# Kernel optimization log

Hardware: AMD Instinct MI355X
Metric: run time of the kernel (lower is better)

## Reference

```python
import jax, jax.numpy as jnp
import numpy as np

B, CIN, COUT, K = 8, 64, 64, 3
H, W = 256, 256
PAD = 1


def setup_inputs() -> dict:
    key = jax.random.key(0)
    k1, k2, k3, k4 = jax.random.split(key, 4)
    x = jax.random.normal(k1, (B, CIN, H, W), dtype=jnp.float32)
    alpha = jax.random.uniform(k2, (B, CIN, 1, 1), dtype=jnp.float32)
    # learned params per init_kwargs (groups=1 -> cin_per_group = CIN)
    weight = jax.random.normal(k3, (1, COUT, CIN, K, K), dtype=jnp.float32) * 0.05
    bias = jax.random.normal(k4, (1, COUT), dtype=jnp.float32) * 0.05
    return {"x": x, "alpha": alpha, "weight": weight, "bias": bias}


def reference(x, alpha, weight, bias):
    # cal_dim='cin': per-sample modulated weights
    # alpha: (B, CIN, 1, 1) -> (B, 1, CIN, 1, 1); weight: (1, COUT, CIN, K, K)
    w = alpha[:, None] * weight  # (B, COUT, CIN, K, K)

    def conv_one(xi, wi):
        # xi: (CIN, H, W), wi: (COUT, CIN, K, K)
        out = jax.lax.conv_general_dilated(
            xi[None], wi,
            window_strides=(1, 1),
            padding=[(PAD, PAD), (PAD, PAD)],
            dimension_numbers=("NCHW", "OIHW", "NCHW"),
        )
        return out[0]  # (COUT, H, W)

    out = jax.vmap(conv_one)(x, w)  # (B, COUT, H, W)
    # bias is repeated per-sample in the torch code -> same bias every sample
    return out + bias[0][None, :, None, None]
```

## Files before the change

### kernel.cpp

```cpp
#include <hip/hip_runtime.h>


typedef __attribute__((ext_vector_type(8))) short short8;
typedef __attribute__((ext_vector_type(4))) float float4v;

#define BB 8
#define CI_N 64
#define CO_N 64
#define HH 256
#define WW 256
#define HW (HH * WW)
#define TW 32
#define TH 8
#define HALO_W 34
#define HALO_H 10
#define HALO_PX (HALO_W * HALO_H)
#define RS 72
#define HI_OFF 32

#define NFRAG (2 * 9 * 2 * 4 * 64 * 8)

__device__ __forceinline__ unsigned f2bf(float v) {
    unsigned u = __float_as_uint(v);
    return (u + 0x7FFFu + ((u >> 16) & 1u)) >> 16;
}

__global__ void prepack_w(const float* __restrict__ w, ushort* __restrict__ wp) {
    int idx = blockIdx.x * 256 + threadIdx.x;
    if (idx >= NFRAG) return;
    int j     = idx & 7;
    int lane  = (idx >> 3) & 63;
    int mt    = (idx >> 9) & 3;
    int plane = (idx >> 11) & 1;
    int rest  = idx >> 12;
    int k     = rest % 9;
    int chunk = rest / 9;
    int co = mt * 16 + (lane & 15);
    int ci = chunk * 32 + (lane >> 4) * 8 + j;
    float v = w[(co * CI_N + ci) * 9 + k];
    unsigned hi = f2bf(v);
    float fhi = __uint_as_float(hi << 16);
    unsigned lo = f2bf(v - fhi);
    wp[idx] = (ushort)(plane ? lo : hi);
}

__global__ __launch_bounds__(512, 4) void conv_mfma(
    const float* __restrict__ x,
    const float* __restrict__ alpha,
    const ushort* __restrict__ wp,
    const float* __restrict__ bias,
    float* __restrict__ out)
{
    __shared__ __align__(16) ushort sx[HALO_PX * RS];

    const int tid    = threadIdx.x;
    const int lane   = tid & 63;
    const int w_id   = tid >> 6;
    const int n_lane = lane & 15;
    const int q      = lane >> 4;

    const int id  = blockIdx.x;
    const int b   = id & 7;
    const int t   = id >> 3;
    const int tx  = t & 7;
    const int ty  = t >> 3;
    const int gx0 = tx * TW;
    const int gy0 = ty * TH;

    const int m_half = w_id >> 2;
    const int n_q    = w_id & 3;

    float4v acc[2][4];
#pragma unroll
    for (int mt = 0; mt < 2; ++mt) {
        float4v bi;
#pragma unroll
        for (int r = 0; r < 4; ++r)
            bi[r] = bias[(m_half * 2 + mt) * 16 + q * 4 + r];
#pragma unroll
        for (int nt = 0; nt < 4; ++nt) acc[mt][nt] = bi;
    }

    const float* xb = x + (size_t)b * CI_N * HW;
    const int vbase = (n_q * 2 * HALO_W + n_lane) * RS + q * 8;

    int gofs[6];
    unsigned okm = 0;
#pragma unroll
    for (int it = 0; it < 6; ++it) {
        int hp = it * 64 + lane;
        int hy = hp / HALO_W;
        int hx = hp - hy * HALO_W;
        int gy = gy0 - 1 + hy;
        int gx = gx0 - 1 + hx;
        bool ok = (hp < HALO_PX) & ((unsigned)gy < HH) & ((unsigned)gx < WW);
        gofs[it] = ok ? gy * WW + gx : 0;
        okm |= (unsigned)ok << it;
    }
    const int cl = w_id * 4;
    float al0[4], al1[4];
#pragma unroll
    for (int j = 0; j < 4; ++j) {
        al0[j] = alpha[b * CI_N + cl + j];
        al1[j] = alpha[b * CI_N + 32 + cl + j];
    }

#define STAGE_LOAD(r, cbase)                                             \
    {                                                                    \
        _Pragma("unroll")                                                \
        for (int j = 0; j < 4; ++j) {                                    \
            const float* xp = xb + (size_t)((cbase) + cl + j) * HW;      \
            _Pragma("unroll")                                            \
            for (int it = 0; it < 6; ++it) r[j][it] = xp[gofs[it]];      \
        }                                                                \
    }

#define STAGE_WRITE(r, al)                                               \
    {                                                                    \
        _Pragma("unroll")                                                \
        for (int it = 0; it < 6; ++it) {                                 \
            if (it < 5 || lane < 20) {         \
                const int hp = it * 64 + lane;                           \
                const bool ok = (okm >> it) & 1;                         \
                float v[4];                                              \
                _Pragma("unroll")                                        \
                for (int j = 0; j < 4; ++j)                              \
                    v[j] = ok ? r[j][it] * al[j] : 0.0f;                 \
                _Pragma("unroll")                                        \
                for (int p2 = 0; p2 < 2; ++p2) {                         \
                    unsigned h0 = f2bf(v[2 * p2]);                       \
                    unsigned h1 = f2bf(v[2 * p2 + 1]);                   \
                    unsigned l0 = f2bf(v[2 * p2]                         \
                                       - __uint_as_float(h0 << 16));     \
                    unsigned l1 = f2bf(v[2 * p2 + 1]                     \
                                       - __uint_as_float(h1 << 16));     \
                    *(unsigned*)&sx[hp * RS + cl + 2 * p2] =             \
                        h0 | (h1 << 16);                                 \
                    *(unsigned*)&sx[hp * RS + HI_OFF + cl + 2 * p2] =    \
                        l0 | (l1 << 16);                                 \
                }                                                        \
            }                                                            \
        }                                                                \
    }

#define COMPUTE(chunk)                                                   \
    {                                                                    \
        _Pragma("unroll")                                                \
        for (int k = 0; k < 9; ++k) {                                    \
            const int dy = k / 3 - 1;                                    \
            const int dx = k % 3 - 1;                                    \
            short8 a_hi[2], a_lo[2];                                     \
            _Pragma("unroll")                                            \
            for (int mt = 0; mt < 2; ++mt) {                             \
                int fh = (((chunk) * 9 + k) * 2 + 0) * 4 + (m_half * 2 + mt); \
                int fl = (((chunk) * 9 + k) * 2 + 1) * 4 + (m_half * 2 + mt); \
                a_hi[mt] = *(const short8*)(wp + (size_t)(fh * 64 + lane) * 8); \
                a_lo[mt] = *(const short8*)(wp + (size_t)(fl * 64 + lane) * 8); \
            }                                                            \
            _Pragma("unroll")                                            \
            for (int nt_i = 0; nt_i < 4; ++nt_i) {                       \
                const int off = ((nt_i >> 1) + 1 + dy) * HALO_W + 1      \
                              + (nt_i & 1) * 16 + dx;                    \
                const ushort* bp = &sx[vbase + off * RS];                \
                short8 b_hi = *(const short8*)bp;                        \
                short8 b_lo = *(const short8*)(bp + HI_OFF);             \
                acc[0][nt_i] = __builtin_amdgcn_mfma_f32_16x16x32_bf16(a_hi[0], b_hi, acc[0][nt_i], 0, 0, 0); \
                acc[1][nt_i] = __builtin_amdgcn_mfma_f32_16x16x32_bf16(a_hi[1], b_hi, acc[1][nt_i], 0, 0, 0); \
                acc[0][nt_i] = __builtin_amdgcn_mfma_f32_16x16x32_bf16(a_lo[0], b_hi, acc[0][nt_i], 0, 0, 0); \
                acc[1][nt_i] = __builtin_amdgcn_mfma_f32_16x16x32_bf16(a_lo[1], b_hi, acc[1][nt_i], 0, 0, 0); \
                acc[0][nt_i] = __builtin_amdgcn_mfma_f32_16x16x32_bf16(a_hi[0], b_lo, acc[0][nt_i], 0, 0, 0); \
                acc[1][nt_i] = __builtin_amdgcn_mfma_f32_16x16x32_bf16(a_hi[1], b_lo, acc[1][nt_i], 0, 0, 0); \
            }                                                            \
        }                                                                \
    }

    float r0[4][6], r1[4][6];
    STAGE_LOAD(r0, 0);
    STAGE_WRITE(r0, al0);
    __syncthreads();

    STAGE_LOAD(r1, 32);
    COMPUTE(0);
    __syncthreads();

    STAGE_WRITE(r1, al1);
    __syncthreads();

    COMPUTE(1);

#pragma unroll
    for (int mt = 0; mt < 2; ++mt) {
        const int m0 = (m_half * 2 + mt) * 16;
#pragma unroll
        for (int nt_i = 0; nt_i < 4; ++nt_i) {
            const int nt = n_q * 4 + nt_i;
            const int gy = gy0 + (nt >> 1);
            const int gx = gx0 + (nt & 1) * 16 + n_lane;
#pragma unroll
            for (int r = 0; r < 4; ++r) {
                const int co = m0 + q * 4 + r;
                out[(((size_t)b * CO_N + co) * HH + gy) * WW + gx] = acc[mt][nt_i][r];
            }
        }
    }
#undef STAGE_LOAD
#undef STAGE_WRITE
#undef COMPUTE
}

extern "C" void kernel_launch(void* const* d_in, const int* in_sizes, int n_in,
                              void* d_out, int out_size, void* d_ws, size_t ws_size,
                              hipStream_t stream) {
    const float* x     = (const float*)d_in[0];
    const float* alpha = (const float*)d_in[1];
    const float* w     = (const float*)d_in[2];
    const float* bias  = (const float*)d_in[3];
    float* out  = (float*)d_out;
    ushort* wpk = (ushort*)d_ws;

    prepack_w<<<dim3((NFRAG + 255) / 256), dim3(256), 0, stream>>>(w, wpk);

    conv_mfma<<<dim3(2048), dim3(512), 0, stream>>>(x, alpha, wpk, bias, out);
}
```

Measured before the change: 334.2 us.

## Make conv blocks persistent over four horizontal tiles with software-pipelined staging

Each block now walks four consecutive 32-wide tiles along a row instead of handling just one, and the grid shrinks from 2048 to 512 blocks. The next tile's first channel half is loaded from global memory while the current tile's second half is computed, so the pipeline spans tile boundaries. This cuts block launch and prologue cost and overlaps loads with MFMA work. In exchange, 512 blocks of 512 threads may underfill the GPU's CUs, and each tile iteration adds extra barriers.

```diff
diff --git a/kernel.cpp b/kernel.cpp
--- a/kernel.cpp
+++ b/kernel.cpp
@@ -61,48 +61,55 @@
 
     const int id  = blockIdx.x;
     const int b   = id & 7;
-    const int t   = id >> 3;
-    const int tx  = t & 7;
-    const int ty  = t >> 3;
-    const int gx0 = tx * TW;
+    const int s   = id >> 3;
+    const int ty  = s >> 1;
+    const int txq = s & 1;
     const int gy0 = ty * TH;
 
     const int m_half = w_id >> 2;
     const int n_q    = w_id & 3;
 
+    float4v bi2[2];
+#pragma unroll
+    for (int mt = 0; mt < 2; ++mt)
+#pragma unroll
+        for (int r = 0; r < 4; ++r)
+            bi2[mt][r] = bias[(m_half * 2 + mt) * 16 + q * 4 + r];
+
     float4v acc[2][4];
 #pragma unroll
-    for (int mt = 0; mt < 2; ++mt) {
-        float4v bi;
-#pragma unroll
-        for (int r = 0; r < 4; ++r)
-            bi[r] = bias[(m_half * 2 + mt) * 16 + q * 4 + r];
-#pragma unroll
-        for (int nt = 0; nt < 4; ++nt) acc[mt][nt] = bi;
-    }
+    for (int mt = 0; mt < 2; ++mt)
+#pragma unroll
+        for (int nt = 0; nt < 4; ++nt) acc[mt][nt] = bi2[mt];
 
     const float* xb = x + (size_t)b * CI_N * HW;
     const int vbase = (n_q * 2 * HALO_W + n_lane) * RS + q * 8;
 
-    int gofs[6];
-    unsigned okm = 0;
-#pragma unroll
-    for (int it = 0; it < 6; ++it) {
-        int hp = it * 64 + lane;
-        int hy = hp / HALO_W;
-        int hx = hp - hy * HALO_W;
-        int gy = gy0 - 1 + hy;
-        int gx = gx0 - 1 + hx;
-        bool ok = (hp < HALO_PX) & ((unsigned)gy < HH) & ((unsigned)gx < WW);
-        gofs[it] = ok ? gy * WW + gx : 0;
-        okm |= (unsigned)ok << it;
-    }
     const int cl = w_id * 4;
     float al0[4], al1[4];
 #pragma unroll
     for (int j = 0; j < 4; ++j) {
         al0[j] = alpha[b * CI_N + cl + j];
         al1[j] = alpha[b * CI_N + 32 + cl + j];
+    }
+
+    int gofs[6];
+    unsigned okm;
+#define CALC_GOFS(gx0_)                                                  \
+    {                                                                    \
+        okm = 0;                                                         \
+        _Pragma("unroll")                                                \
+        for (int it = 0; it < 6; ++it) {                                 \
+            int hp = it * 64 + lane;                                     \
+            int hy = hp / HALO_W;                                        \
+            int hx = hp - hy * HALO_W;                                   \
+            int gy = gy0 - 1 + hy;                                       \
+            int gx = (gx0_)-1 + hx;                                      \
+            bool ok = (hp < HALO_PX) & ((unsigned)gy < HH)               \
+                    & ((unsigned)gx < WW);                               \
+            gofs[it] = ok ? gy * WW + gx : 0;                            \
+            okm |= (unsigned)ok << it;                                   \
+        }                                                                \
     }
 
 #define STAGE_LOAD(r, cbase)                                             \
@@ -174,35 +181,52 @@
         }                                                                \
     }
 
-    float r0[4][6], r1[4][6];
-    STAGE_LOAD(r0, 0);
-    STAGE_WRITE(r0, al0);
+    int gx0 = txq * 4 * TW;
+    float r[4][6];
+    CALC_GOFS(gx0);
+    STAGE_LOAD(r, 0);
+    STAGE_WRITE(r, al0);
     __syncthreads();
 
-    STAGE_LOAD(r1, 32);
-    COMPUTE(0);
-    __syncthreads();
-
-    STAGE_WRITE(r1, al1);
-    __syncthreads();
-
-    COMPUTE(1);
-
-#pragma unroll
-    for (int mt = 0; mt < 2; ++mt) {
-        const int m0 = (m_half * 2 + mt) * 16;
-#pragma unroll
-        for (int nt_i = 0; nt_i < 4; ++nt_i) {
-            const int nt = n_q * 4 + nt_i;
-            const int gy = gy0 + (nt >> 1);
-            const int gx = gx0 + (nt & 1) * 16 + n_lane;
-#pragma unroll
-            for (int r = 0; r < 4; ++r) {
-                const int co = m0 + q * 4 + r;
-                out[(((size_t)b * CO_N + co) * HH + gy) * WW + gx] = acc[mt][nt_i][r];
+#pragma unroll 1
+    for (int ti = 0; ti < 4; ++ti) {
+        STAGE_LOAD(r, 32);
+        COMPUTE(0);
+        __syncthreads();
+        STAGE_WRITE(r, al1);
+        __syncthreads();
+
+        const int egx0 = gx0;
+        if (ti < 3) {
+            gx0 += TW;
+            CALC_GOFS(gx0);
+            STAGE_LOAD(r, 0);
+        }
+        COMPUTE(1);
+
+#pragma unroll
+        for (int mt = 0; mt < 2; ++mt) {
+            const int m0 = (m_half * 2 + mt) * 16;
+#pragma unroll
+            for (int nt_i = 0; nt_i < 4; ++nt_i) {
+                const int nt = n_q * 4 + nt_i;
+                const int gy = gy0 + (nt >> 1);
+                const int gx = egx0 + (nt & 1) * 16 + n_lane;
+#pragma unroll
+                for (int rr = 0; rr < 4; ++rr) {
+                    const int co = m0 + q * 4 + rr;
+                    out[(((size_t)b * CO_N + co) * HH + gy) * WW + gx] = acc[mt][nt_i][rr];
+                }
+                acc[mt][nt_i] = bi2[mt];
             }
         }
-    }
+        __syncthreads();
+        if (ti < 3) {
+            STAGE_WRITE(r, al0);
+            __syncthreads();
+        }
+    }
+#undef CALC_GOFS
 #undef STAGE_LOAD
 #undef STAGE_WRITE
 #undef COMPUTE
@@ -220,5 +244,5 @@
 
     prepack_w<<<dim3((NFRAG + 255) / 256), dim3(256), 0, stream>>>(w, wpk);
 
-    conv_mfma<<<dim3(2048), dim3(512), 0, stream>>>(x, alpha, wpk, bias, out);
-}
+    conv_mfma<<<dim3(512), dim3(512), 0, stream>>>(x, alpha, wpk, bias, out);
+}
```

Measured after the change: 766.3 us. +129.3%, slower.

## Halve conv tile height and double-buffer LDS to drop a barrier

Applied to the files above, without the earlier changes.

Shrinks the spatial tile from 32x8 to 32x4 pixels and doubles the grid, so each wave handles one output row of two 16-pixel fragments. Splits the shared halo buffer into two buffers so the second channel chunk can be written while the first is still being read, removing one __syncthreads. The cost is a larger halo-to-output ratio, which means more redundant global x reads and weight-fragment loads per MFMA. Two LDS buffers also raise shared memory per block, which may lower the number of resident blocks per CU.

```diff
diff --git a/kernel.cpp b/kernel.cpp
--- a/kernel.cpp
+++ b/kernel.cpp
@@ -11,9 +11,9 @@
 #define WW 256
 #define HW (HH * WW)
 #define TW 32
-#define TH 8
+#define TH 4
 #define HALO_W 34
-#define HALO_H 10
+#define HALO_H 6
 #define HALO_PX (HALO_W * HALO_H)
 #define RS 72
 #define HI_OFF 32
@@ -51,7 +51,8 @@
     const float* __restrict__ bias,
     float* __restrict__ out)
 {
-    __shared__ __align__(16) ushort sx[HALO_PX * RS];
+    __shared__ __align__(16) ushort sxA[HALO_PX * RS];
+    __shared__ __align__(16) ushort sxB[HALO_PX * RS];
 
     const int tid    = threadIdx.x;
     const int lane   = tid & 63;
@@ -70,7 +71,7 @@
     const int m_half = w_id >> 2;
     const int n_q    = w_id & 3;
 
-    float4v acc[2][4];
+    float4v acc[2][2];
 #pragma unroll
     for (int mt = 0; mt < 2; ++mt) {
         float4v bi;
@@ -78,16 +79,16 @@
         for (int r = 0; r < 4; ++r)
             bi[r] = bias[(m_half * 2 + mt) * 16 + q * 4 + r];
 #pragma unroll
-        for (int nt = 0; nt < 4; ++nt) acc[mt][nt] = bi;
+        for (int h = 0; h < 2; ++h) acc[mt][h] = bi;
     }
 
     const float* xb = x + (size_t)b * CI_N * HW;
-    const int vbase = (n_q * 2 * HALO_W + n_lane) * RS + q * 8;
-
-    int gofs[6];
+    const int vbase = n_lane * RS + q * 8;
+
+    int gofs[4];
     unsigned okm = 0;
 #pragma unroll
-    for (int it = 0; it < 6; ++it) {
+    for (int it = 0; it < 4; ++it) {
         int hp = it * 64 + lane;
         int hy = hp / HALO_W;
         int hx = hp - hy * HALO_W;
@@ -111,15 +112,15 @@
         for (int j = 0; j < 4; ++j) {                                    \
             const float* xp = xb + (size_t)((cbase) + cl + j) * HW;      \
             _Pragma("unroll")                                            \
-            for (int it = 0; it < 6; ++it) r[j][it] = xp[gofs[it]];      \
+            for (int it = 0; it < 4; ++it) r[j][it] = xp[gofs[it]];      \
         }                                                                \
     }
 
-#define STAGE_WRITE(r, al)                                               \
+#define STAGE_WRITE(buf, r, al)                                          \
     {                                                                    \
         _Pragma("unroll")                                                \
-        for (int it = 0; it < 6; ++it) {                                 \
-            if (it < 5 || lane < 20) {         \
+        for (int it = 0; it < 4; ++it) {                                 \
+            if (it < 3 || lane < 12) {         \
                 const int hp = it * 64 + lane;                           \
                 const bool ok = (okm >> it) & 1;                         \
                 float v[4];                                              \
@@ -134,16 +135,16 @@
                                        - __uint_as_float(h0 << 16));     \
                     unsigned l1 = f2bf(v[2 * p2 + 1]                     \
                                        - __uint_as_float(h1 << 16));     \
-                    *(unsigned*)&sx[hp * RS + cl + 2 * p2] =             \
+                    *(unsigned*)&buf[hp * RS + cl + 2 * p2] =            \
                         h0 | (h1 << 16);                                 \
-                    *(unsigned*)&sx[hp * RS + HI_OFF + cl + 2 * p2] =    \
+                    *(unsigned*)&buf[hp * RS + HI_OFF + cl + 2 * p2] =   \
                         l0 | (l1 << 16);                                 \
                 }                                                        \
             }                                                            \
         }                                                                \
     }
 
-#define COMPUTE(chunk)                                                   \
+#define COMPUTE(chunk, buf)                                              \
     {                                                                    \
         _Pragma("unroll")                                                \
         for (int k = 0; k < 9; ++k) {                                    \
@@ -158,48 +159,44 @@
                 a_lo[mt] = *(const short8*)(wp + (size_t)(fl * 64 + lane) * 8); \
             }                                                            \
             _Pragma("unroll")                                            \
-            for (int nt_i = 0; nt_i < 4; ++nt_i) {                       \
-                const int off = ((nt_i >> 1) + 1 + dy) * HALO_W + 1      \
-                              + (nt_i & 1) * 16 + dx;                    \
-                const ushort* bp = &sx[vbase + off * RS];                \
+            for (int h = 0; h < 2; ++h) {                                \
+                const int off = (n_q + 1 + dy) * HALO_W + 1 + h * 16 + dx; \
+                const ushort* bp = &buf[vbase + off * RS];               \
                 short8 b_hi = *(const short8*)bp;                        \
                 short8 b_lo = *(const short8*)(bp + HI_OFF);             \
-                acc[0][nt_i] = __builtin_amdgcn_mfma_f32_16x16x32_bf16(a_hi[0], b_hi, acc[0][nt_i], 0, 0, 0); \
-                acc[1][nt_i] = __builtin_amdgcn_mfma_f32_16x16x32_bf16(a_hi[1], b_hi, acc[1][nt_i], 0, 0, 0); \
-                acc[0][nt_i] = __builtin_amdgcn_mfma_f32_16x16x32_bf16(a_lo[0], b_hi, acc[0][nt_i], 0, 0, 0); \
-                acc[1][nt_i] = __builtin_amdgcn_mfma_f32_16x16x32_bf16(a_lo[1], b_hi, acc[1][nt_i], 0, 0, 0); \
-                acc[0][nt_i] = __builtin_amdgcn_mfma_f32_16x16x32_bf16(a_hi[0], b_lo, acc[0][nt_i], 0, 0, 0); \
-                acc[1][nt_i] = __builtin_amdgcn_mfma_f32_16x16x32_bf16(a_hi[1], b_lo, acc[1][nt_i], 0, 0, 0); \
+                acc[0][h] = __builtin_amdgcn_mfma_f32_16x16x32_bf16(a_hi[0], b_hi, acc[0][h], 0, 0, 0); \
+                acc[1][h] = __builtin_amdgcn_mfma_f32_16x16x32_bf16(a_hi[1], b_hi, acc[1][h], 0, 0, 0); \
+                acc[0][h] = __builtin_amdgcn_mfma_f32_16x16x32_bf16(a_lo[0], b_hi, acc[0][h], 0, 0, 0); \
+                acc[1][h] = __builtin_amdgcn_mfma_f32_16x16x32_bf16(a_lo[1], b_hi, acc[1][h], 0, 0, 0); \
+                acc[0][h] = __builtin_amdgcn_mfma_f32_16x16x32_bf16(a_hi[0], b_lo, acc[0][h], 0, 0, 0); \
+                acc[1][h] = __builtin_amdgcn_mfma_f32_16x16x32_bf16(a_hi[1], b_lo, acc[1][h], 0, 0, 0); \
             }                                                            \
         }                                                                \
     }
 
-    float r0[4][6], r1[4][6];
+    float r0[4][4], r1[4][4];
     STAGE_LOAD(r0, 0);
-    STAGE_WRITE(r0, al0);
+    STAGE_WRITE(sxA, r0, al0);
     __syncthreads();
 
     STAGE_LOAD(r1, 32);
-    COMPUTE(0);
+    COMPUTE(0, sxA);
+    STAGE_WRITE(sxB, r1, al1);
     __syncthreads();
 
-    STAGE_WRITE(r1, al1);
-    __syncthreads();
-
-    COMPUTE(1);
+    COMPUTE(1, sxB);
 
 #pragma unroll
     for (int mt = 0; mt < 2; ++mt) {
         const int m0 = (m_half * 2 + mt) * 16;
 #pragma unroll
-        for (int nt_i = 0; nt_i < 4; ++nt_i) {
-            const int nt = n_q * 4 + nt_i;
-            const int gy = gy0 + (nt >> 1);
-            const int gx = gx0 + (nt & 1) * 16 + n_lane;
+        for (int h = 0; h < 2; ++h) {
+            const int gy = gy0 + n_q;
+            const int gx = gx0 + h * 16 + n_lane;
 #pragma unroll
             for (int r = 0; r < 4; ++r) {
                 const int co = m0 + q * 4 + r;
-                out[(((size_t)b * CO_N + co) * HH + gy) * WW + gx] = acc[mt][nt_i][r];
+                out[(((size_t)b * CO_N + co) * HH + gy) * WW + gx] = acc[mt][h][r];
             }
         }
     }
@@ -220,5 +217,5 @@
 
     prepack_w<<<dim3((NFRAG + 255) / 256), dim3(256), 0, stream>>>(w, wpk);
 
-    conv_mfma<<<dim3(2048), dim3(512), 0, stream>>>(x, alpha, wpk, bias, out);
-}
+    conv_mfma<<<dim3(4096), dim3(512), 0, stream>>>(x, alpha, wpk, bias, out);
+}
```

Result: no change. 332.6 us (-0.5%).
